# Kernel optimization log

Measured on AMD Instinct MI355X. Metric: run time of the kernel, lower is better.

Reference implementation:

```python
import jax, jax.numpy as jnp
import numpy as np

B, L, H, D, HEADS = 8, 1024, 768, 64, 12


def _sincos(seq_len, d):
    # sinusoid table pe[pos, 2i]=sin(pos/10000^(2i/d)), pe[pos,2i+1]=cos(...)
    # RoPE uses sin = pe[:, ::2] repeat_interleave(2), cos = pe[:, 1::2] repeat_interleave(2)
    pos = jnp.arange(seq_len, dtype=jnp.float32)[:, None]           # (L,1)
    i = jnp.arange(d // 2, dtype=jnp.float32)
    ang = pos * jnp.power(10000.0, -2.0 * i / d)                     # (L, d/2)
    sin = jnp.repeat(jnp.sin(ang), 2, axis=-1)                       # (L, d)
    cos = jnp.repeat(jnp.cos(ang), 2, axis=-1)                       # (L, d)
    return sin, cos


def _rope(x, sin, cos):
    # x: (b, l, d); rotate pairs: x2 = [-x1, x0, -x3, x2, ...]
    x2 = jnp.stack([-x[..., 1::2], x[..., ::2]], axis=-1).reshape(x.shape)
    return x * cos + x2 * sin


def setup_inputs() -> dict:
    key = jax.random.key(0)
    ks = jax.random.split(key, 5)
    return {
        "hidden_state": jax.random.normal(ks[0], (B, L, H), dtype=jnp.float32),
        "mask": jnp.ones((B, L), dtype=jnp.int32),
        "W1": jax.random.normal(ks[1], (H, 2 * D), dtype=jnp.float32) * 0.02,
        "b1": jnp.zeros((2 * D,), dtype=jnp.float32),
        "W2": jax.random.normal(ks[2], (2 * D, 2 * HEADS), dtype=jnp.float32) * 0.02,
        "b2": jnp.zeros((2 * HEADS,), dtype=jnp.float32),
    }


def reference(hidden_state, mask, W1, b1, W2, b2):
    b, l, _ = hidden_state.shape
    seq = hidden_state @ W1 + b1                                     # (b, l, 2D)
    qw, kw = seq[..., :D], seq[..., D:]                              # (b, l, D)
    sin, cos = _sincos(l, D)
    qw = _rope(qw, sin, cos)
    kw = _rope(kw, sin, cos)
    logits = jnp.einsum('bmd,bnd->bmn', qw, kw) / (D ** 0.5)         # (b, l, l)
    bias = (seq @ W2 + b2).reshape(b, l, HEADS, 2).transpose(0, 2, 1, 3)  # (b, heads, l, 2)
    logits = logits[:, None] + bias[..., :1] + bias[..., 1:].swapaxes(2, 3)  # (b, heads, l, l)
    m = mask.astype(bool)
    neg_inf = jnp.array(-jnp.inf, logits.dtype)
    logits = jnp.where(m[:, None, :, None], logits, neg_inf)
    logits = jnp.where(m[:, None, None, :], logits, neg_inf)
    tri = jnp.tril(jnp.ones((l, l), logits.dtype), -1)
    logits = logits - tri * jnp.array(1e12, logits.dtype)
    return logits
```

## Files before the change

kernel.cpp:

```cpp
#include <hip/hip_runtime.h>
#include <math.h>

#define HDIM 768
#define DD 64
#define SEQL 1024
#define NH 12
#define NB 8

__global__ __launch_bounds__(128) void k1_seq_rope_bias(
    const float* __restrict__ hidden, const float* __restrict__ W1,
    const float* __restrict__ b1, const float* __restrict__ W2,
    const float* __restrict__ b2,
    float* __restrict__ qo, float* __restrict__ ko,
    float* __restrict__ bqo, float* __restrict__ bko)
{
    __shared__ float hs[16 * HDIM];
    __shared__ float sq[16][132];
    const int tid = threadIdx.x;
    const long row0 = (long)blockIdx.x * 16;

    const float4* src = (const float4*)(hidden + row0 * HDIM);
    float4* hdst = (float4*)hs;
    #pragma unroll
    for (int t = 0; t < 24; ++t)
        hdst[tid + t * 128] = src[tid + t * 128];
    __syncthreads();

    const int cx = tid & 31;
    const int ry = tid >> 5;
    const float4 bias1 = ((const float4*)b1)[cx];
    float4 acc[4];
    #pragma unroll
    for (int r = 0; r < 4; ++r) acc[r] = bias1;

    for (int k4 = 0; k4 < HDIM / 4; ++k4) {
        float4 w[4];
        #pragma unroll
        for (int kk = 0; kk < 4; ++kk)
            w[kk] = *(const float4*)(W1 + (k4 * 4 + kk) * 128 + cx * 4);
        #pragma unroll
        for (int r = 0; r < 4; ++r) {
            float4 hv = *(const float4*)(hs + (ry * 4 + r) * HDIM + k4 * 4);
            acc[r].x = fmaf(hv.x, w[0].x, fmaf(hv.y, w[1].x, fmaf(hv.z, w[2].x, fmaf(hv.w, w[3].x, acc[r].x))));
            acc[r].y = fmaf(hv.x, w[0].y, fmaf(hv.y, w[1].y, fmaf(hv.z, w[2].y, fmaf(hv.w, w[3].y, acc[r].y))));
            acc[r].z = fmaf(hv.x, w[0].z, fmaf(hv.y, w[1].z, fmaf(hv.z, w[2].z, fmaf(hv.w, w[3].z, acc[r].z))));
            acc[r].w = fmaf(hv.x, w[0].w, fmaf(hv.y, w[1].w, fmaf(hv.z, w[2].w, fmaf(hv.w, w[3].w, acc[r].w))));
        }
    }
    #pragma unroll
    for (int r = 0; r < 4; ++r)
        *(float4*)&sq[ry * 4 + r][cx * 4] = acc[r];
    __syncthreads();

    for (int idx = tid; idx < 16 * 24; idx += 128) {
        int r = idx / 24, jj = idx - r * 24;
        float s = b2[jj];
        #pragma unroll 16
        for (int c = 0; c < 128; ++c)
            s = fmaf(sq[r][c], W2[c * 24 + jj], s);
        long grow = row0 + r;
        if (jj & 1) bko[grow * NH + (jj >> 1)] = s;
        else        bqo[grow * NH + (jj >> 1)] = s;
    }

    for (int idx = tid; idx < 16 * 32; idx += 128) {
        int r = idx >> 5, p = idx & 31;
        long grow = row0 + r;
        int pos = (int)(grow & (SEQL - 1));
        float inv = __expf((float)p * -0.28782313662425576f);
        float ang = (float)pos * inv;
        float sn, cs;
        __sincosf(ang, &sn, &cs);
        long base = grow * DD;
        float x0 = sq[r][2 * p], x1 = sq[r][2 * p + 1];
        qo[base + 2 * p]     = x0 * cs - x1 * sn;
        qo[base + 2 * p + 1] = x1 * cs + x0 * sn;
        float y0 = sq[r][DD + 2 * p], y1 = sq[r][DD + 2 * p + 1];
        ko[base + 2 * p]     = y0 * cs - y1 * sn;
        ko[base + 2 * p + 1] = y1 * cs + y0 * sn;
    }
}

__global__ __launch_bounds__(256, 2) void k2_logits(
    const float* __restrict__ q, const float* __restrict__ kmat,
    const float* __restrict__ bq, const float* __restrict__ bk,
    const int* __restrict__ mask, float* __restrict__ out)
{
    __shared__ float qs[128][68];
    __shared__ float ks[64][68];
    const int tid = threadIdx.x;
    const int b = blockIdx.z;
    const int m0 = blockIdx.y * 128;
    const int n0 = blockIdx.x * 64;

    const float4* qsrc = (const float4*)(q + ((long)b * SEQL + m0) * DD);
    #pragma unroll
    for (int t = 0; t < 8; ++t) {
        int idx = tid + t * 256;
        *(float4*)&qs[idx >> 4][(idx & 15) * 4] = qsrc[idx];
    }
    const float4* ksrc = (const float4*)(kmat + ((long)b * SEQL + n0) * DD);
    #pragma unroll
    for (int t = 0; t < 4; ++t) {
        int idx = tid + t * 256;
        *(float4*)&ks[idx >> 4][(idx & 15) * 4] = ksrc[idx];
    }
    __syncthreads();

    const int tm = tid >> 4;
    const int tn = tid & 15;
    float acc[8][4];
    #pragma unroll
    for (int i = 0; i < 8; ++i)
        #pragma unroll
        for (int j = 0; j < 4; ++j) acc[i][j] = 0.f;

    #pragma unroll
    for (int k4 = 0; k4 < 16; ++k4) {
        float4 kv[4];
        #pragma unroll
        for (int j = 0; j < 4; ++j)
            kv[j] = *(const float4*)&ks[tn + 16 * j][k4 * 4];
        #pragma unroll
        for (int i = 0; i < 8; ++i) {
            float4 qv = *(const float4*)&qs[tm + 16 * i][k4 * 4];
            #pragma unroll
            for (int j = 0; j < 4; ++j)
                acc[i][j] = fmaf(qv.x, kv[j].x, fmaf(qv.y, kv[j].y,
                             fmaf(qv.z, kv[j].z, fmaf(qv.w, kv[j].w, acc[i][j]))));
        }
    }

    int mm[8], mn[4];
    #pragma unroll
    for (int i = 0; i < 8; ++i) mm[i] = mask[b * SEQL + m0 + tm + 16 * i];
    #pragma unroll
    for (int j = 0; j < 4; ++j) mn[j] = mask[b * SEQL + n0 + tn + 16 * j];
    #pragma unroll
    for (int i = 0; i < 8; ++i) {
        int m = m0 + tm + 16 * i;
        #pragma unroll
        for (int j = 0; j < 4; ++j) {
            int n = n0 + tn + 16 * j;
            float v = acc[i][j] * 0.125f;
            if (m > n) v -= 1e12f;
            if (!(mm[i] && mn[j])) v = -INFINITY;
            acc[i][j] = v;
        }
    }

    #pragma unroll 1
    for (int h = 0; h < NH; ++h) {
        float bkv[4];
        #pragma unroll
        for (int j = 0; j < 4; ++j)
            bkv[j] = bk[(long)(b * SEQL + n0 + tn + 16 * j) * NH + h];
        float* ob = out + ((long)(b * NH + h) * SEQL + m0) * SEQL + n0 + tn;
        #pragma unroll
        for (int i = 0; i < 8; ++i) {
            float bqv = bq[(long)(b * SEQL + m0 + tm + 16 * i) * NH + h];
            float* rp = ob + (long)(tm + 16 * i) * SEQL;
            #pragma unroll
            for (int j = 0; j < 4; ++j)
                rp[16 * j] = acc[i][j] + bqv + bkv[j];
        }
    }
}

extern "C" void kernel_launch(void* const* d_in, const int* in_sizes, int n_in,
                              void* d_out, int out_size, void* d_ws, size_t ws_size,
                              hipStream_t stream) {
    const float* hidden = (const float*)d_in[0];
    const int*   mask   = (const int*)d_in[1];
    const float* W1     = (const float*)d_in[2];
    const float* b1     = (const float*)d_in[3];
    const float* W2     = (const float*)d_in[4];
    const float* b2     = (const float*)d_in[5];
    float* out = (float*)d_out;

    float* ws = (float*)d_ws;
    float* qbuf  = ws;
    float* kbuf  = qbuf + (long)NB * SEQL * DD;
    float* bqbuf = kbuf + (long)NB * SEQL * DD;
    float* bkbuf = bqbuf + (long)NB * SEQL * NH;

    k1_seq_rope_bias<<<512, 128, 0, stream>>>(hidden, W1, b1, W2, b2,
                                              qbuf, kbuf, bqbuf, bkbuf);
    k2_logits<<<dim3(16, 8, 8), 256, 0, stream>>>(qbuf, kbuf, bqbuf, bkbuf, mask, out);
}
```

Baseline: 159.5 us.

## Vectorize logits stores with contiguous column mapping and stage biases in LDS

Each thread now owns four adjacent output columns rather than columns strided by 16, so every output row segment goes out as a single 128-bit nontemporal store. The per-head bq/bk bias values are staged once in shared memory, replacing repeated global loads inside the head loop, and the column mask is read as one int4. The aim is to cut store instruction count and cache pollution on the write-bound 400MB output. The K tile row pitch changes to 65 floats, which makes the float4 LDS reads unaligned and may add bank conflicts or misaligned-access cost.

Measured after the change: 132.2 us. 17.1% less time.

```diff
diff --git a/kernel.cpp b/kernel.cpp
--- a/kernel.cpp
+++ b/kernel.cpp
@@ -6,6 +6,8 @@
 #define SEQL 1024
 #define NH 12
 #define NB 8
+
+typedef float f32x4 __attribute__((ext_vector_type(4)));
 
 __global__ __launch_bounds__(128) void k1_seq_rope_bias(
     const float* __restrict__ hidden, const float* __restrict__ W1,
@@ -87,7 +89,9 @@
     const int* __restrict__ mask, float* __restrict__ out)
 {
     __shared__ float qs[128][68];
-    __shared__ float ks[64][68];
+    __shared__ float ks[64][65];
+    __shared__ float bqs[128][13];
+    __shared__ float bks[64][13];
     const int tid = threadIdx.x;
     const int b = blockIdx.z;
     const int m0 = blockIdx.y * 128;
@@ -105,6 +109,18 @@
         int idx = tid + t * 256;
         *(float4*)&ks[idx >> 4][(idx & 15) * 4] = ksrc[idx];
     }
+    const float* bqg = bq + (long)(b * SEQL + m0) * NH;
+    #pragma unroll
+    for (int t = 0; t < 6; ++t) {
+        int idx = tid + t * 256;
+        bqs[idx / 12][idx % 12] = bqg[idx];
+    }
+    const float* bkg = bk + (long)(b * SEQL + n0) * NH;
+    #pragma unroll
+    for (int t = 0; t < 3; ++t) {
+        int idx = tid + t * 256;
+        bks[idx / 12][idx % 12] = bkg[idx];
+    }
     __syncthreads();
 
     const int tm = tid >> 4;
@@ -120,7 +136,7 @@
         float4 kv[4];
         #pragma unroll
         for (int j = 0; j < 4; ++j)
-            kv[j] = *(const float4*)&ks[tn + 16 * j][k4 * 4];
+            kv[j] = *(const float4*)&ks[4 * tn + j][k4 * 4];
         #pragma unroll
         for (int i = 0; i < 8; ++i) {
             float4 qv = *(const float4*)&qs[tm + 16 * i][k4 * 4];
@@ -131,17 +147,17 @@
         }
     }
 
-    int mm[8], mn[4];
+    int mm[8];
     #pragma unroll
     for (int i = 0; i < 8; ++i) mm[i] = mask[b * SEQL + m0 + tm + 16 * i];
-    #pragma unroll
-    for (int j = 0; j < 4; ++j) mn[j] = mask[b * SEQL + n0 + tn + 16 * j];
+    const int4 mn4 = *(const int4*)(mask + b * SEQL + n0 + 4 * tn);
+    int mn[4] = {mn4.x, mn4.y, mn4.z, mn4.w};
     #pragma unroll
     for (int i = 0; i < 8; ++i) {
         int m = m0 + tm + 16 * i;
         #pragma unroll
         for (int j = 0; j < 4; ++j) {
-            int n = n0 + tn + 16 * j;
+            int n = n0 + 4 * tn + j;
             float v = acc[i][j] * 0.125f;
             if (m > n) v -= 1e12f;
             if (!(mm[i] && mn[j])) v = -INFINITY;
@@ -154,15 +170,17 @@
         float bkv[4];
         #pragma unroll
         for (int j = 0; j < 4; ++j)
-            bkv[j] = bk[(long)(b * SEQL + n0 + tn + 16 * j) * NH + h];
-        float* ob = out + ((long)(b * NH + h) * SEQL + m0) * SEQL + n0 + tn;
+            bkv[j] = bks[4 * tn + j][h];
+        float* ob = out + ((long)(b * NH + h) * SEQL + m0) * SEQL + n0 + 4 * tn;
         #pragma unroll
         for (int i = 0; i < 8; ++i) {
-            float bqv = bq[(long)(b * SEQL + m0 + tm + 16 * i) * NH + h];
-            float* rp = ob + (long)(tm + 16 * i) * SEQL;
-            #pragma unroll
-            for (int j = 0; j < 4; ++j)
-                rp[16 * j] = acc[i][j] + bqv + bkv[j];
+            float bqv = bqs[tm + 16 * i][h];
+            f32x4 v;
+            v.x = acc[i][0] + bqv + bkv[0];
+            v.y = acc[i][1] + bqv + bkv[1];
+            v.z = acc[i][2] + bqv + bkv[2];
+            v.w = acc[i][3] + bqv + bkv[3];
+            __builtin_nontemporal_store(v, (f32x4*)(ob + (long)(tm + 16 * i) * SEQL));
         }
     }
 }
```

## Retile logits kernel for float4 nontemporal stores and staged bias tables

Applied to the files above, without the earlier changes.

The logits kernel now uses 32x256 tiles. K is staged transposed in shared memory so each lane owns four consecutive columns and writes one float4 per row with a nontemporal store, replacing the strided scalar stores. The per-head bq/bk bias values are preloaded into shared memory instead of being gathered from global memory inside the head loop, and the mask columns are read as int4. The aim is to cut the cost of the large output write, in exchange for more shared memory per block and a transposing K load with scalar LDS writes.

New measurement: 132.5 us. 1.2x faster.

```diff
diff --git a/kernel.cpp b/kernel.cpp
--- a/kernel.cpp
+++ b/kernel.cpp
@@ -6,6 +6,8 @@
 #define SEQL 1024
 #define NH 12
 #define NB 8
+
+typedef float f32x4 __attribute__((ext_vector_type(4)));
 
 __global__ __launch_bounds__(128) void k1_seq_rope_bias(
     const float* __restrict__ hidden, const float* __restrict__ W1,
@@ -81,88 +83,96 @@
     }
 }
 
-__global__ __launch_bounds__(256, 2) void k2_logits(
+__global__ __launch_bounds__(256) void k2_logits(
     const float* __restrict__ q, const float* __restrict__ kmat,
     const float* __restrict__ bq, const float* __restrict__ bk,
     const int* __restrict__ mask, float* __restrict__ out)
 {
-    __shared__ float qs[128][68];
-    __shared__ float ks[64][68];
+    __shared__ float qs[32][64];
+    __shared__ float kst[64][256];
+    __shared__ float bqs[32][12];
+    __shared__ float bkst[12][256];
     const int tid = threadIdx.x;
+    const int lane = tid & 63;
+    const int wv = tid >> 6;
     const int b = blockIdx.z;
-    const int m0 = blockIdx.y * 128;
-    const int n0 = blockIdx.x * 64;
+    const int m0 = blockIdx.y * 32;
+    const int n0 = blockIdx.x * 256;
 
     const float4* qsrc = (const float4*)(q + ((long)b * SEQL + m0) * DD);
-    #pragma unroll
-    for (int t = 0; t < 8; ++t) {
-        int idx = tid + t * 256;
-        *(float4*)&qs[idx >> 4][(idx & 15) * 4] = qsrc[idx];
-    }
-    const float4* ksrc = (const float4*)(kmat + ((long)b * SEQL + n0) * DD);
-    #pragma unroll
-    for (int t = 0; t < 4; ++t) {
-        int idx = tid + t * 256;
-        *(float4*)&ks[idx >> 4][(idx & 15) * 4] = ksrc[idx];
+    ((float4*)qs)[tid]       = qsrc[tid];
+    ((float4*)qs)[tid + 256] = qsrc[tid + 256];
+
+    const float4* ksrc = (const float4*)(kmat + ((long)b * SEQL + n0 + tid) * DD);
+    #pragma unroll
+    for (int t = 0; t < 16; ++t) {
+        float4 kv = ksrc[t];
+        kst[t * 4 + 0][tid] = kv.x;
+        kst[t * 4 + 1][tid] = kv.y;
+        kst[t * 4 + 2][tid] = kv.z;
+        kst[t * 4 + 3][tid] = kv.w;
+    }
+
+    if (tid < 96)
+        ((float4*)bqs)[tid] = ((const float4*)(bq + ((long)b * SEQL + m0) * NH))[tid];
+
+    {
+        const float4* bsrc = (const float4*)(bk + ((long)b * SEQL + n0 + tid) * NH);
+        float4 v0 = bsrc[0], v1 = bsrc[1], v2 = bsrc[2];
+        bkst[0][tid] = v0.x; bkst[1][tid]  = v0.y; bkst[2][tid]  = v0.z; bkst[3][tid]  = v0.w;
+        bkst[4][tid] = v1.x; bkst[5][tid]  = v1.y; bkst[6][tid]  = v1.z; bkst[7][tid]  = v1.w;
+        bkst[8][tid] = v2.x; bkst[9][tid]  = v2.y; bkst[10][tid] = v2.z; bkst[11][tid] = v2.w;
     }
     __syncthreads();
 
-    const int tm = tid >> 4;
-    const int tn = tid & 15;
-    float acc[8][4];
-    #pragma unroll
-    for (int i = 0; i < 8; ++i)
-        #pragma unroll
-        for (int j = 0; j < 4; ++j) acc[i][j] = 0.f;
+    const int r0 = wv * 8;
+    f32x4 acc[8];
+    #pragma unroll
+    for (int i = 0; i < 8; ++i) acc[i] = 0.f;
 
     #pragma unroll
     for (int k4 = 0; k4 < 16; ++k4) {
-        float4 kv[4];
-        #pragma unroll
-        for (int j = 0; j < 4; ++j)
-            kv[j] = *(const float4*)&ks[tn + 16 * j][k4 * 4];
+        f32x4 kv0 = *(const f32x4*)&kst[4 * k4 + 0][4 * lane];
+        f32x4 kv1 = *(const f32x4*)&kst[4 * k4 + 1][4 * lane];
+        f32x4 kv2 = *(const f32x4*)&kst[4 * k4 + 2][4 * lane];
+        f32x4 kv3 = *(const f32x4*)&kst[4 * k4 + 3][4 * lane];
         #pragma unroll
         for (int i = 0; i < 8; ++i) {
-            float4 qv = *(const float4*)&qs[tm + 16 * i][k4 * 4];
-            #pragma unroll
-            for (int j = 0; j < 4; ++j)
-                acc[i][j] = fmaf(qv.x, kv[j].x, fmaf(qv.y, kv[j].y,
-                             fmaf(qv.z, kv[j].z, fmaf(qv.w, kv[j].w, acc[i][j]))));
-        }
-    }
-
-    int mm[8], mn[4];
-    #pragma unroll
-    for (int i = 0; i < 8; ++i) mm[i] = mask[b * SEQL + m0 + tm + 16 * i];
-    #pragma unroll
-    for (int j = 0; j < 4; ++j) mn[j] = mask[b * SEQL + n0 + tn + 16 * j];
+            const f32x4 qv = *(const f32x4*)&qs[r0 + i][4 * k4];
+            acc[i] += qv.x * kv0;
+            acc[i] += qv.y * kv1;
+            acc[i] += qv.z * kv2;
+            acc[i] += qv.w * kv3;
+        }
+    }
+
+    int mrow[8];
+    #pragma unroll
+    for (int i = 0; i < 8; ++i) mrow[i] = mask[b * SEQL + m0 + r0 + i];
+    const int4 mn4 = *(const int4*)(mask + b * SEQL + n0 + 4 * lane);
+    const int mn[4] = {mn4.x, mn4.y, mn4.z, mn4.w};
+    const int nb = n0 + 4 * lane;
     #pragma unroll
     for (int i = 0; i < 8; ++i) {
-        int m = m0 + tm + 16 * i;
+        const int m = m0 + r0 + i;
         #pragma unroll
         for (int j = 0; j < 4; ++j) {
-            int n = n0 + tn + 16 * j;
             float v = acc[i][j] * 0.125f;
-            if (m > n) v -= 1e12f;
-            if (!(mm[i] && mn[j])) v = -INFINITY;
+            if (m > nb + j) v -= 1e12f;
+            if (!(mrow[i] && mn[j])) v = -INFINITY;
             acc[i][j] = v;
         }
     }
 
     #pragma unroll 1
     for (int h = 0; h < NH; ++h) {
-        float bkv[4];
-        #pragma unroll
-        for (int j = 0; j < 4; ++j)
-            bkv[j] = bk[(long)(b * SEQL + n0 + tn + 16 * j) * NH + h];
-        float* ob = out + ((long)(b * NH + h) * SEQL + m0) * SEQL + n0 + tn;
+        const f32x4 bkv = *(const f32x4*)&bkst[h][4 * lane];
+        float* ob = out + ((long)(b * NH + h) << 20) + ((long)(m0 + r0) << 10) + nb;
         #pragma unroll
         for (int i = 0; i < 8; ++i) {
-            float bqv = bq[(long)(b * SEQL + m0 + tm + 16 * i) * NH + h];
-            float* rp = ob + (long)(tm + 16 * i) * SEQL;
-            #pragma unroll
-            for (int j = 0; j < 4; ++j)
-                rp[16 * j] = acc[i][j] + bqv + bkv[j];
+            const float bqv = bqs[r0 + i][h];
+            f32x4 v = acc[i] + bqv + bkv;
+            __builtin_nontemporal_store(v, (f32x4*)(ob + ((long)i << 10)));
         }
     }
 }
@@ -186,5 +196,5 @@
 
     k1_seq_rope_bias<<<512, 128, 0, stream>>>(hidden, W1, b1, W2, b2,
                                               qbuf, kbuf, bqbuf, bkbuf);
-    k2_logits<<<dim3(16, 8, 8), 256, 0, stream>>>(qbuf, kbuf, bqbuf, bkbuf, mask, out);
+    k2_logits<<<dim3(4, 32, 8), 256, 0, stream>>>(qbuf, kbuf, bqbuf, bkbuf, mask, out);
 }
```
